# Kernel optimization log

Hardware: AMD Instinct MI355X
Metric: run time of the kernel (lower is better)

## Reference

```python
import jax, jax.numpy as jnp
import numpy as np

B, S, H = 2, 256, 256
R = H  # rdim defaults to hidden_size


def setup_inputs() -> dict:
    key = jax.random.key(0)
    k1, k2, k3 = jax.random.split(key, 3)
    hidden_states = jax.random.normal(k1, (B, S, H), dtype=jnp.float32)
    # Linear weights stored torch-style [out, in]
    Wqkv = jax.random.normal(k2, (3 * R, H), dtype=jnp.float32) * (H ** -0.5)
    bqkv = jnp.zeros((3 * R,), dtype=jnp.float32)
    Wc = jax.random.normal(k3, (R, R), dtype=jnp.float32) * (R ** -0.5)
    bc = jnp.zeros((R,), dtype=jnp.float32)
    return {"hidden_states": hidden_states, "Wqkv": Wqkv, "bqkv": bqkv, "Wc": Wc, "bc": bc}


def reference(hidden_states, Wqkv, bqkv, Wc, bc):
    # qkv projection: [B,S,3R]
    qkv = jnp.einsum('bsh,rh->bsr', hidden_states, Wqkv) + bqkv
    q, k, v = jnp.split(qkv, 3, axis=-1)  # each [B,S,R]
    # Tucker-style outer-product scores: [B,S,L,R]
    scores = jnp.einsum('bsr,blr->bslr', q, k)
    # c_proj mixes the r dimension
    scores = jnp.einsum('bslr,pr->bslp', scores, Wc) + bc
    # rearrange 'b s l r -> (b r) s l' + softmax(dim=-1) == softmax over l axis
    probs = jax.nn.softmax(scores, axis=2)
    # 'brsl,blr->bsr' after rearrange back == 'bslr,blr->bsr'
    return jnp.einsum('bslr,blr->bsr', probs, v)
```

## Files before the change

### kernel.cpp

```cpp
#include <hip/hip_runtime.h>
#include <hip/hip_bf16.h>
#include <math.h>

typedef __bf16 bf16;
typedef _Float16 f16;
typedef __attribute__((ext_vector_type(8))) __bf16 bf16x8;
typedef __attribute__((ext_vector_type(8))) _Float16 f16x8;
typedef __attribute__((ext_vector_type(4))) _Float16 f16x4;
typedef __attribute__((ext_vector_type(4))) float floatx4;

#define MFMA16(a, b, c) __builtin_amdgcn_mfma_f32_16x16x16f16(a, b, c, 0, 0, 0)

__device__ __forceinline__ void split8(floatx4 a0, floatx4 a1, bf16x8& hi, bf16x8& lo) {
#pragma unroll
    for (int t = 0; t < 4; t++) {
        float v0 = a0[t], v1 = a1[t];
        bf16 h0 = (bf16)v0, h1 = (bf16)v1;
        hi[t] = h0;     lo[t] = (bf16)(v0 - (float)h0);
        hi[t + 4] = h1; lo[t + 4] = (bf16)(v1 - (float)h1);
    }
}

__global__ __launch_bounds__(256, 4)
void proj_kernel(const float* __restrict__ hs, const float* __restrict__ Wq,
                 const float* __restrict__ bq, const float* __restrict__ Wc,
                 f16* __restrict__ q_ws, f16* __restrict__ k_ws,
                 f16* __restrict__ vT_ws, f16* __restrict__ Wc_ws)
{
    const int tid = threadIdx.x;
    if (blockIdx.x >= 384) {
        const int base = (blockIdx.x - 384) * 1024 + tid * 4;
        floatx4 w = *(const floatx4*)(Wc + base);
        f16x4 h;
        h.x = (f16)w.x; h.y = (f16)w.y; h.z = (f16)w.z; h.w = (f16)w.w;
        *(f16x4*)(Wc_ws + base) = h;
        return;
    }
    const int wv = tid >> 6, lane = tid & 63;
    const int quad = lane >> 4, lcol = lane & 15;
    const int wt = blockIdx.x * 4 + wv;
    const int rt = wt / 48, ct = wt - rt * 48;
    const int row0 = rt * 16, col0 = ct * 16;

    const float* arow = hs + (row0 + lcol) * 256;
    const float* brow = Wq + (col0 + lcol) * 256;

    floatx4 acc = {0.f, 0.f, 0.f, 0.f};
#pragma unroll
    for (int ks = 0; ks < 8; ks++) {
        const int h = ks * 32 + quad * 8;
        floatx4 a0 = *(const floatx4*)(arow + h);
        floatx4 a1 = *(const floatx4*)(arow + h + 4);
        floatx4 b0 = *(const floatx4*)(brow + h);
        floatx4 b1 = *(const floatx4*)(brow + h + 4);
        bf16x8 ahi, alo, bhi, blo;
        split8(a0, a1, ahi, alo);
        split8(b0, b1, bhi, blo);
        acc = __builtin_amdgcn_mfma_f32_16x16x32_bf16(ahi, bhi, acc, 0, 0, 0);
        acc = __builtin_amdgcn_mfma_f32_16x16x32_bf16(ahi, blo, acc, 0, 0, 0);
        acc = __builtin_amdgcn_mfma_f32_16x16x32_bf16(alo, bhi, acc, 0, 0, 0);
    }
    const float bias = bq[col0 + lcol];
    const int col = col0 + lcol, seg = col0 >> 8, jj = col & 255;
#pragma unroll
    for (int r = 0; r < 4; r++) {
        const int row = row0 + quad * 4 + r;
        const float val = acc[r] + bias;
        if (seg == 0)      q_ws[row * 256 + jj] = (f16)val;
        else if (seg == 1) k_ws[row * 256 + jj] = (f16)val;
        else               vT_ws[(row >> 8) * 65536 + jj * 256 + (row & 255)] = (f16)val;
    }
}

__global__ __launch_bounds__(512, 2)
void attn_main(const f16* __restrict__ qw, const f16* __restrict__ kw,
               const f16* __restrict__ vT, const f16* __restrict__ Wc16,
               float* __restrict__ out)
{
    __shared__ f16 Klds[256 * 256];
    __shared__ f16 Plds[8 * 64 * 24];
    __shared__ float obuf[4][2][64];
    __shared__ float sbuf[4][2][64];

    const int bid = blockIdx.x;
    const int pt = bid & 3;
    const int sg = (bid >> 2) & 31;
    const int b  = bid >> 7;
    const int p0 = pt * 64;
    const int tid  = threadIdx.x;
    const int wv   = tid >> 6;
    const int lane = tid & 63;
    const int quad = lane >> 4, lcol = lane & 15;
    const int lq = wv & 3, sh = wv >> 2;
    const int l0w = lq * 64;

    const f16* kbase = kw + b * 65536;
    const f16* vbase = vT + b * 65536;

#pragma unroll
    for (int it = 0; it < 16; it++) {
        const int id = tid + it * 512;
        const int l = id >> 5, c = id & 31;
        const int csrc = c ^ (l & 7);
        uint4 d = *(const uint4*)(kbase + l * 256 + csrc * 8);
        *(uint4*)(Klds + l * 256 + c * 8) = d;
    }

    f16x4 vfrag[4][4];
#pragma unroll
    for (int d = 0; d < 4; d++)
#pragma unroll
        for (int c = 0; c < 4; c++)
            vfrag[d][c] = *(const f16x4*)(vbase + (p0 + d * 16 + lcol) * 256 + l0w + c * 16 + quad * 4);

    f16x4 ones4;
#pragma unroll
    for (int t = 0; t < 4; t++) ones4[t] = (f16)1.0f;

    __syncthreads();

    f16* Pw = Plds + wv * 1536;

    for (int sl = 0; sl < 4; sl++) {
        const int s = sg * 8 + sh * 4 + sl;
        const f16* qrow = qw + (b * 256 + s) * 256;

        floatx4 acc[4][4];
#pragma unroll
        for (int i = 0; i < 4; i++)
#pragma unroll
            for (int j = 0; j < 4; j++)
                acc[i][j] = (floatx4){0.f, 0.f, 0.f, 0.f};

#pragma unroll
        for (int kk = 0; kk < 8; kk++) {
            const int rb = kk * 32 + quad * 8;
            f16x8 qv = *(const f16x8*)(qrow + rb);
            f16x8 kf[4];
#pragma unroll
            for (int i = 0; i < 4; i++)
                kf[i] = *(const f16x8*)(Klds + (l0w + i * 16 + lcol) * 256 +
                                        (((kk * 4 + quad) ^ (lcol & 7)) << 3));
#pragma unroll
            for (int j = 0; j < 4; j++) {
                f16x8 wv8 = *(const f16x8*)(Wc16 + (p0 + j * 16 + lcol) * 256 + rb);
                f16x8 bf = wv8 * qv;
#pragma unroll
                for (int i = 0; i < 4; i++)
                    acc[i][j] = __builtin_amdgcn_mfma_f32_16x16x32_f16(kf[i], bf, acc[i][j], 0, 0, 0);
            }
        }

        floatx4 co[4], cs[4];
#pragma unroll
        for (int d = 0; d < 4; d++) {
            co[d] = (floatx4){0.f, 0.f, 0.f, 0.f};
            cs[d] = (floatx4){0.f, 0.f, 0.f, 0.f};
        }
#pragma unroll
        for (int c = 0; c < 4; c++) {
#pragma unroll
            for (int j = 0; j < 4; j++) {
                f16x4 pv;
#pragma unroll
                for (int r = 0; r < 4; r++)
                    pv[r] = (f16)__expf(acc[c][j][r]);
                *(f16x4*)(Pw + (j * 16 + lcol) * 24 + quad * 4) = pv;
            }
#pragma unroll
            for (int d = 0; d < 4; d++) {
                f16x4 pa = *(const f16x4*)(Pw + (d * 16 + lcol) * 24 + quad * 4);
                co[d] = MFMA16(pa, vfrag[d][c], co[d]);
                cs[d] = MFMA16(pa, ones4, cs[d]);
            }
        }

        if ((lcol >> 2) == quad) {
            const int r = lcol & 3;
#pragma unroll
            for (int d = 0; d < 4; d++) {
                obuf[lq][sh][d * 16 + lcol] = co[d][r];
                sbuf[lq][sh][d * 16 + lcol] = cs[d][r];
            }
        }
        __syncthreads();
        if (tid < 128) {
            const int ss = tid >> 6, p = tid & 63;
            const float O = obuf[0][ss][p] + obuf[1][ss][p] + obuf[2][ss][p] + obuf[3][ss][p];
            const float S = sbuf[0][ss][p] + sbuf[1][ss][p] + sbuf[2][ss][p] + sbuf[3][ss][p];
            out[(b * 256 + sg * 8 + ss * 4 + sl) * 256 + p0 + p] = O / S;
        }
        __syncthreads();
    }
}

extern "C" void kernel_launch(void* const* d_in, const int* in_sizes, int n_in,
                              void* d_out, int out_size, void* d_ws, size_t ws_size,
                              hipStream_t stream) {
    const float* hs   = (const float*)d_in[0];
    const float* Wqkv = (const float*)d_in[1];
    const float* bqkv = (const float*)d_in[2];
    const float* Wc   = (const float*)d_in[3];
    float* out = (float*)d_out;

    char* ws = (char*)d_ws;
    f16* q_ws   = (f16*)ws;
    f16* k_ws   = (f16*)(ws + 262144);
    f16* vT_ws  = (f16*)(ws + 524288);
    f16* Wc_ws  = (f16*)(ws + 786432);

    proj_kernel<<<dim3(448), 256, 0, stream>>>(hs, Wqkv, bqkv, Wc, q_ws, k_ws, vT_ws, Wc_ws);
    attn_main<<<dim3(256), 512, 0, stream>>>(q_ws, k_ws, vT_ws, Wc_ws, out);
}
```

Baseline: 107.8 us.

## Double attention block to 1024 threads and drop LDS transpose of probabilities

The attention kernel now runs 16 waves per block, each owning 32 l-rows instead of 64, which halves the per-wave accumulator footprint and raises the number of waves in flight. The probability-times-V step no longer round-trips through shared memory. It swaps MFMA operand order so exp'd scores feed the B operand directly. The softmax denominator is computed with lane shuffles instead of an extra MFMA against ones. The costs are a larger 8-way cross-wave reduction and a launch bound of 1024 threads that caps registers per thread.

```diff
diff --git a/kernel.cpp b/kernel.cpp
--- a/kernel.cpp
+++ b/kernel.cpp
@@ -72,15 +72,14 @@
     }
 }
 
-__global__ __launch_bounds__(512, 2)
+__global__ __launch_bounds__(1024, 4)
 void attn_main(const f16* __restrict__ qw, const f16* __restrict__ kw,
                const f16* __restrict__ vT, const f16* __restrict__ Wc16,
                float* __restrict__ out)
 {
     __shared__ f16 Klds[256 * 256];
-    __shared__ f16 Plds[8 * 64 * 24];
-    __shared__ float obuf[4][2][64];
-    __shared__ float sbuf[4][2][64];
+    __shared__ float obuf[2][8][64];
+    __shared__ float sbuf[2][8][64];
 
     const int bid = blockIdx.x;
     const int pt = bid & 3;
@@ -91,43 +90,38 @@
     const int wv   = tid >> 6;
     const int lane = tid & 63;
     const int quad = lane >> 4, lcol = lane & 15;
-    const int lq = wv & 3, sh = wv >> 2;
-    const int l0w = lq * 64;
+    const int sh = wv >> 3;
+    const int lo = wv & 7;
+    const int l0 = lo * 32;
 
     const f16* kbase = kw + b * 65536;
     const f16* vbase = vT + b * 65536;
 
 #pragma unroll
-    for (int it = 0; it < 16; it++) {
-        const int id = tid + it * 512;
+    for (int it = 0; it < 8; it++) {
+        const int id = tid + it * 1024;
         const int l = id >> 5, c = id & 31;
         const int csrc = c ^ (l & 7);
         uint4 d = *(const uint4*)(kbase + l * 256 + csrc * 8);
         *(uint4*)(Klds + l * 256 + c * 8) = d;
     }
 
-    f16x4 vfrag[4][4];
-#pragma unroll
-    for (int d = 0; d < 4; d++)
-#pragma unroll
-        for (int c = 0; c < 4; c++)
-            vfrag[d][c] = *(const f16x4*)(vbase + (p0 + d * 16 + lcol) * 256 + l0w + c * 16 + quad * 4);
-
-    f16x4 ones4;
-#pragma unroll
-    for (int t = 0; t < 4; t++) ones4[t] = (f16)1.0f;
+    f16x4 vfragA[4][2];
+#pragma unroll
+    for (int j = 0; j < 4; j++)
+#pragma unroll
+        for (int i = 0; i < 2; i++)
+            vfragA[j][i] = *(const f16x4*)(vbase + (p0 + j * 16 + lcol) * 256 + l0 + i * 16 + quad * 4);
 
     __syncthreads();
-
-    f16* Pw = Plds + wv * 1536;
 
     for (int sl = 0; sl < 4; sl++) {
         const int s = sg * 8 + sh * 4 + sl;
         const f16* qrow = qw + (b * 256 + s) * 256;
 
-        floatx4 acc[4][4];
-#pragma unroll
-        for (int i = 0; i < 4; i++)
+        floatx4 acc[2][4];
+#pragma unroll
+        for (int i = 0; i < 2; i++)
 #pragma unroll
             for (int j = 0; j < 4; j++)
                 acc[i][j] = (floatx4){0.f, 0.f, 0.f, 0.f};
@@ -136,58 +130,51 @@
         for (int kk = 0; kk < 8; kk++) {
             const int rb = kk * 32 + quad * 8;
             f16x8 qv = *(const f16x8*)(qrow + rb);
-            f16x8 kf[4];
-#pragma unroll
-            for (int i = 0; i < 4; i++)
-                kf[i] = *(const f16x8*)(Klds + (l0w + i * 16 + lcol) * 256 +
+            f16x8 kf[2];
+#pragma unroll
+            for (int i = 0; i < 2; i++)
+                kf[i] = *(const f16x8*)(Klds + (l0 + i * 16 + lcol) * 256 +
                                         (((kk * 4 + quad) ^ (lcol & 7)) << 3));
 #pragma unroll
             for (int j = 0; j < 4; j++) {
                 f16x8 wv8 = *(const f16x8*)(Wc16 + (p0 + j * 16 + lcol) * 256 + rb);
                 f16x8 bf = wv8 * qv;
-#pragma unroll
-                for (int i = 0; i < 4; i++)
-                    acc[i][j] = __builtin_amdgcn_mfma_f32_16x16x32_f16(kf[i], bf, acc[i][j], 0, 0, 0);
+                acc[0][j] = __builtin_amdgcn_mfma_f32_16x16x32_f16(kf[0], bf, acc[0][j], 0, 0, 0);
+                acc[1][j] = __builtin_amdgcn_mfma_f32_16x16x32_f16(kf[1], bf, acc[1][j], 0, 0, 0);
             }
         }
 
-        floatx4 co[4], cs[4];
-#pragma unroll
-        for (int d = 0; d < 4; d++) {
-            co[d] = (floatx4){0.f, 0.f, 0.f, 0.f};
-            cs[d] = (floatx4){0.f, 0.f, 0.f, 0.f};
-        }
-#pragma unroll
-        for (int c = 0; c < 4; c++) {
-#pragma unroll
-            for (int j = 0; j < 4; j++) {
-                f16x4 pv;
-#pragma unroll
-                for (int r = 0; r < 4; r++)
-                    pv[r] = (f16)__expf(acc[c][j][r]);
-                *(f16x4*)(Pw + (j * 16 + lcol) * 24 + quad * 4) = pv;
-            }
-#pragma unroll
-            for (int d = 0; d < 4; d++) {
-                f16x4 pa = *(const f16x4*)(Pw + (d * 16 + lcol) * 24 + quad * 4);
-                co[d] = MFMA16(pa, vfrag[d][c], co[d]);
-                cs[d] = MFMA16(pa, ones4, cs[d]);
-            }
-        }
-
-        if ((lcol >> 2) == quad) {
-            const int r = lcol & 3;
-#pragma unroll
-            for (int d = 0; d < 4; d++) {
-                obuf[lq][sh][d * 16 + lcol] = co[d][r];
-                sbuf[lq][sh][d * 16 + lcol] = cs[d][r];
+#pragma unroll
+        for (int j = 0; j < 4; j++) {
+            floatx4 co = {0.f, 0.f, 0.f, 0.f};
+            float ssj = 0.f;
+#pragma unroll
+            for (int i = 0; i < 2; i++) {
+                f16x4 pb;
+#pragma unroll
+                for (int t = 0; t < 4; t++) {
+                    float e = __expf(acc[i][j][t]);
+                    pb[t] = (f16)e;
+                    ssj += e;
+                }
+                co = MFMA16(vfragA[j][i], pb, co);
+            }
+            ssj += __shfl_xor(ssj, 16);
+            ssj += __shfl_xor(ssj, 32);
+            if (quad == (lcol >> 2)) {
+                obuf[sh][lo][j * 16 + lcol] = co[lcol & 3];
+                sbuf[sh][lo][j * 16 + lcol] = ssj;
             }
         }
         __syncthreads();
         if (tid < 128) {
             const int ss = tid >> 6, p = tid & 63;
-            const float O = obuf[0][ss][p] + obuf[1][ss][p] + obuf[2][ss][p] + obuf[3][ss][p];
-            const float S = sbuf[0][ss][p] + sbuf[1][ss][p] + sbuf[2][ss][p] + sbuf[3][ss][p];
+            float O = 0.f, S = 0.f;
+#pragma unroll
+            for (int o = 0; o < 8; o++) {
+                O += obuf[ss][o][p];
+                S += sbuf[ss][o][p];
+            }
             out[(b * 256 + sg * 8 + ss * 4 + sl) * 256 + p0 + p] = O / S;
         }
         __syncthreads();
@@ -210,5 +197,5 @@
     f16* Wc_ws  = (f16*)(ws + 786432);
 
     proj_kernel<<<dim3(448), 256, 0, stream>>>(hs, Wqkv, bqkv, Wc, q_ws, k_ws, vT_ws, Wc_ws);
-    attn_main<<<dim3(256), 512, 0, stream>>>(q_ws, k_ws, vT_ws, Wc_ws, out);
-}
+    attn_main<<<dim3(256), 1024, 0, stream>>>(q_ws, k_ws, vT_ws, Wc_ws, out);
+}
```

After: 160.9 us. 1.49x slower.
